# Kernel tuning notes

Measured on AMD Instinct MI355X. Metric: run time of the kernel, lower is better.

## Reference

```python
import jax, jax.numpy as jnp
import numpy as np

D_Z, D_X, K, T = 128, 64, 16, 2048
JITTER = 1e-4
# Tsit5 Butcher tableau. diffrax.diffeqsolve with the default ConstantStepSize
# controller and dt0 = t_curr - t_prev takes exactly ONE Tsit5 step per interval,
# so a single explicit Tsit5 step reproduces the original math.
A21 = 0.161
A31, A32 = -0.008480655492356989, 0.335480655492357
A41, A42, A43 = 2.8971530571054935, -6.359448489975075, 4.3622954328695815
A51, A52, A53, A54 = 5.325864828439257, -11.748883564062828, 7.4955393428898365, -0.09249506636175525
A61, A62, A63, A64, A65 = 5.86145544294642, -12.92096931784711, 8.159367898576159, -0.071584973281401, -0.028269050394068383
B1, B2, B3, B4, B5, B6 = 0.09646076681806523, 0.01, 0.4798896504144996, 1.379008574103742, -3.290069515436081, 2.324710524099774


def setup_inputs() -> dict:
    key = jax.random.key(0)
    ks = jax.random.split(key, 8)
    xs = jax.random.normal(ks[0], (T, D_X), jnp.float32)
    ts = jnp.arange(T, dtype=jnp.float32) * 0.01  # strictly increasing observation times
    expected_s = jax.nn.softmax(jax.random.normal(ks[1], (T, K), jnp.float32), axis=-1)
    mu_0 = jax.random.normal(ks[2], (D_Z,), jnp.float32)
    P_0 = jnp.eye(D_Z, dtype=jnp.float32)
    # stable continuous dynamics: small random part, negative diagonal shift
    A_s = 0.02 * jax.random.normal(ks[3], (K, D_Z, D_Z), jnp.float32) - 0.5 * jnp.eye(D_Z, dtype=jnp.float32)
    b_s = 0.1 * jax.random.normal(ks[4], (K, D_Z), jnp.float32)
    Q_s_chol = 0.1 + 0.1 * jax.random.uniform(ks[5], (K, D_Z), dtype=jnp.float32)
    C = jax.random.normal(ks[6], (D_X, D_Z), jnp.float32) / jnp.sqrt(jnp.float32(D_Z))
    R = 0.1 * jnp.eye(D_X, dtype=jnp.float32)
    return dict(xs=xs, ts=ts, expected_s=expected_s, mu_0=mu_0, P_0=P_0,
                A_s=A_s, b_s=b_s, Q_s_chol=Q_s_chol, C=C, R=R)


def _ode_func(state, s_prob, A_s, b_s, Q_s_chol):
    # state packs [mu (D_Z), P.flatten() (D_Z*D_Z)]
    mu, P = state[:D_Z], state[D_Z:].reshape(D_Z, D_Z)
    w = s_prob / jnp.sum(s_prob)  # jnp.average(..., weights=s_prob) semantics
    drift = jnp.einsum('k,kij,j->i', w, A_s, mu) + w @ b_s
    eA = jnp.einsum('k,kij->ij', w, A_s)
    eQ = jnp.diag(w @ (Q_s_chol ** 2))  # weighted avg of diag(Q_chol)^2
    dP = eA @ P + P @ eA.T + eQ
    return jnp.concatenate([drift, dP.reshape(-1)])


def _kf_update(mu, P, x, C, R):
    y = x - C @ mu
    S = C @ P @ C.T + R + JITTER * jnp.eye(R.shape[0], dtype=P.dtype)
    cho = jax.scipy.linalg.cho_factor(S)
    Kg = jax.scipy.linalg.cho_solve(cho, C @ P).T
    mu_u = mu + Kg @ y
    P_u = P - Kg @ C @ P
    return mu_u, 0.5 * (P_u + P_u.T)


def reference(xs, ts, expected_s, mu_0, P_0, A_s, b_s, Q_s_chol, C, R):
    mu0u, P0u = _kf_update(mu_0, P_0, xs[0], C, R)

    def step(carry, inp):
        mu_prev, P_prev, t_prev = carry
        x, t, s = inp
        y0 = jnp.concatenate([mu_prev, P_prev.reshape(-1)])
        f = lambda st: _ode_func(st, s, A_s, b_s, Q_s_chol)

        def integrate(_):
            h = t - t_prev
            k1 = f(y0)
            k2 = f(y0 + h * (A21 * k1))
            k3 = f(y0 + h * (A31 * k1 + A32 * k2))
            k4 = f(y0 + h * (A41 * k1 + A42 * k2 + A43 * k3))
            k5 = f(y0 + h * (A51 * k1 + A52 * k2 + A53 * k3 + A54 * k4))
            k6 = f(y0 + h * (A61 * k1 + A62 * k2 + A63 * k3 + A64 * k4 + A65 * k5))
            return y0 + h * (B1 * k1 + B2 * k2 + B3 * k3 + B4 * k4 + B5 * k5 + B6 * k6)

        state_pred = jax.lax.cond(t > t_prev, integrate, lambda _: y0, None)
        mu_pr, P_pr = state_pred[:D_Z], state_pred[D_Z:].reshape(D_Z, D_Z)
        mu_u, P_u = _kf_update(mu_pr, P_pr, x, C, R)
        return (mu_u, P_u, t), (mu_u, P_u)

    _, (mu_f, P_f) = jax.lax.scan(step, (mu0u, P0u, ts[0]), (xs[1:], ts[1:], expected_s[1:]))
    mu_filt = jnp.concatenate([mu0u[None], mu_f], axis=0)  # (T, D_Z)
    P_filt = jnp.concatenate([P0u[None], P_f], axis=0)  # (T, D_Z, D_Z)
    return mu_filt, P_filt
```

## Files before the change

### kernel.cpp

```cpp
#include <hip/hip_runtime.h>
#include <math.h>

#define DZ 128
#define DX 64
#define KMIX 16
#define JITTER_C 1e-4f
#define MS (DZ*DZ)
#define ESZ (4*MS + 2*DZ)
#define NCH 256
#define NT 1024
#define SCN (5*MS + 256)

#define SP   0
#define SX   (1*MS)
#define SX2  (2*MS)
#define SX2T (3*MS)
#define SQ   (4*MS)

template<int M, int N, int K, int MODE, bool DUAL>
__device__ void mm_(const float* __restrict__ At, const float* __restrict__ B,
                    float* __restrict__ out, const float* __restrict__ aux,
                    float* __restrict__ outT, float e1 = 0.f)
{
    __syncthreads();
    const int tid = threadIdx.x;
    constexpr int TM = M/32, TN = N/32;
    const int tx = tid & 31, ty = tid >> 5;
    const int i0 = ty*TM, j0 = tx*TN;
    float acc[TM*TN];
#pragma unroll
    for (int e = 0; e < TM*TN; ++e) acc[e] = 0.f;
#pragma unroll 8
    for (int k = 0; k < K; ++k) {
        const float* ar = At + k*M + i0;
        const float* br = B + k*N + j0;
        float av[TM], bv[TN];
        if constexpr (TM == 2) {
            float2 t = *reinterpret_cast<const float2*>(ar);
            av[0]=t.x; av[1]=t.y;
        } else {
#pragma unroll
            for (int a = 0; a < TM; a += 4) {
                float4 t = *reinterpret_cast<const float4*>(ar + a);
                av[a]=t.x; av[a+1]=t.y; av[a+2]=t.z; av[a+3]=t.w;
            }
        }
        if constexpr (TN == 2) {
            float2 t = *reinterpret_cast<const float2*>(br);
            bv[0]=t.x; bv[1]=t.y;
        } else {
#pragma unroll
            for (int b = 0; b < TN; b += 4) {
                float4 t = *reinterpret_cast<const float4*>(br + b);
                bv[b]=t.x; bv[b+1]=t.y; bv[b+2]=t.z; bv[b+3]=t.w;
            }
        }
#pragma unroll
        for (int a = 0; a < TM; ++a)
#pragma unroll
            for (int b = 0; b < TN; ++b)
                acc[a*TN+b] = fmaf(av[a], bv[b], acc[a*TN+b]);
    }
#pragma unroll
    for (int a = 0; a < TM; ++a) {
#pragma unroll
        for (int b = 0; b < TN; ++b) {
            const int row = i0+a, col = j0+b;
            const int idx = row*N + col;
            float v = acc[a*TN+b];
            if constexpr (MODE == 1) v += out[idx];
            else if constexpr (MODE == 2) v = aux[idx] - v;
            else if constexpr (MODE == 3) v += aux[idx];
            else if constexpr (MODE == 4) { v += e1*aux[idx]; if (row==col) v += 1.f; }
            out[idx] = v;
            acc[a*TN+b] = v;
        }
    }
    if constexpr (DUAL) {
#pragma unroll
        for (int b = 0; b < TN; ++b) {
#pragma unroll
            for (int a = 0; a < TM; a += 4) {
                float4 v = make_float4(acc[(a)*TN+b], acc[(a+1)*TN+b], acc[(a+2)*TN+b], acc[(a+3)*TN+b]);
                *reinterpret_cast<float4*>(outT + (j0+b)*M + i0 + a) = v;
            }
        }
    }
    __syncthreads();
}

template<int M, int K, int MODE>
__device__ void mv_(const float* __restrict__ At, const float* __restrict__ v,
                    float* __restrict__ out, const float* __restrict__ aux)
{
    __syncthreads();
    const int tid = threadIdx.x;
    if (tid < M) {
        float s = 0.f;
        for (int k = 0; k < K; ++k)
            s = fmaf(At[k*M + tid], v[k], s);
        float r;
        if constexpr (MODE == 0) r = s;
        else if constexpr (MODE == 1) r = aux[tid] + s;
        else r = aux[tid] - s;
        out[tid] = r;
    }
    __syncthreads();
}

__device__ void trans_g(const float* __restrict__ src, float* __restrict__ dst,
                        float* __restrict__ Lb)
{
    __syncthreads();
    for (int e = threadIdx.x; e < MS; e += NT) Lb[e] = src[e];
    __syncthreads();
    for (int e = threadIdx.x; e < MS; e += NT) {
        int j = e >> 7, i = e & 127;
        dst[e] = Lb[i*DZ + j];
    }
    __syncthreads();
}

__device__ void gj64_spd(float* __restrict__ A, float* __restrict__ st)
{
    const int tid = threadIdx.x;
    for (int p = 0; p < DX; p += 4) {
        __syncthreads();
        if (tid < 64) {
#pragma unroll
            for (int b = 0; b < 4; ++b) st[tid*4+b] = A[tid*DX + p + b];
        } else if (tid < 128) {
            int j = tid - 64;
#pragma unroll
            for (int b = 0; b < 4; ++b) st[256 + b*64 + j] = A[(p+b)*DX + j];
        }
        __syncthreads();
        float Dm[16], Di[16];
#pragma unroll
        for (int a = 0; a < 4; ++a)
#pragma unroll
            for (int b = 0; b < 4; ++b) {
                Dm[a*4+b] = st[(p+a)*4 + b];
                Di[a*4+b] = (a==b) ? 1.f : 0.f;
            }
#pragma unroll
        for (int q = 0; q < 4; ++q) {
            float rp = 1.f / Dm[q*4+q];
#pragma unroll
            for (int j = 0; j < 4; ++j) { Dm[q*4+j] *= rp; Di[q*4+j] *= rp; }
#pragma unroll
            for (int i = 0; i < 4; ++i) {
                if (i == q) continue;
                float f = Dm[i*4+q];
#pragma unroll
                for (int j = 0; j < 4; ++j) { Dm[i*4+j] = fmaf(-f, Dm[q*4+j], Dm[i*4+j]); Di[i*4+j] = fmaf(-f, Di[q*4+j], Di[i*4+j]); }
            }
        }
        for (int e = tid; e < DX*DX; e += NT) {
            const int i = e >> 6, j = e & 63;
            const bool iP = (i >= p) && (i < p+4);
            const bool jP = (j >= p) && (j < p+4);
            float o;
            if (iP && jP) {
                o = Di[(i-p)*4 + (j-p)];
            } else if (iP) {
                const int a = i - p;
                o = Di[a*4+0]*st[256+0*64+j] + Di[a*4+1]*st[256+1*64+j]
                  + Di[a*4+2]*st[256+2*64+j] + Di[a*4+3]*st[256+3*64+j];
            } else {
                float Ei[4];
#pragma unroll
                for (int b = 0; b < 4; ++b)
                    Ei[b] = st[i*4+0]*Di[0*4+b] + st[i*4+1]*Di[1*4+b]
                          + st[i*4+2]*Di[2*4+b] + st[i*4+3]*Di[3*4+b];
                if (jP) o = -Ei[j-p];
                else    o = A[e] - (Ei[0]*st[256+0*64+j] + Ei[1]*st[256+1*64+j]
                                  + Ei[2]*st[256+2*64+j] + Ei[3]*st[256+3*64+j]);
            }
            A[e] = o;
        }
    }
    __syncthreads();
}

__device__ void gj128_piv(float* __restrict__ A, float* __restrict__ pc, float* __restrict__ pr,
                          int* __restrict__ rec, int* __restrict__ ipv1)
{
    __syncthreads();
    const int tid = threadIdx.x;
    for (int p = 0; p < DZ; ++p) {
        if (tid < 64) {
            float best = -1.f; int bi = p;
            for (int i = tid; i < DZ; i += 64) {
                float v = (i >= p) ? fabsf(A[i*DZ + p]) : -2.f;
                if (v > best) { best = v; bi = i; }
            }
            for (int off = 32; off > 0; off >>= 1) {
                float ob = __shfl_xor(best, off);
                int obi = __shfl_xor(bi, off);
                if (ob > best) { best = ob; bi = obi; }
            }
            if (tid == 0) { rec[p] = bi; ipv1[0] = bi; }
        }
        __syncthreads();
        const int r = ipv1[0];
        if (r != p) {
            for (int j = tid; j < DZ; j += NT) { float t = A[p*DZ+j]; A[p*DZ+j] = A[r*DZ+j]; A[r*DZ+j] = t; }
            __syncthreads();
        }
        if (tid < DZ) { pc[tid] = A[tid*DZ + p]; pr[tid] = A[p*DZ + tid]; }
        __syncthreads();
        const float rp = 1.f / pr[p];
        for (int e = tid; e < MS; e += NT) {
            const int i = e >> 7, j = e & 127;
            const float pv = pr[j] * rp;
            float o;
            if (i == p) o = (j == p) ? rp : pv;
            else { const float fc = pc[i]; o = (j == p) ? (-fc*rp) : (A[e] - fc*pv); }
            A[e] = o;
        }
        __syncthreads();
    }
    for (int p = DZ - 1; p >= 0; --p) {
        const int r = rec[p];
        if (r != p) {
            for (int i = tid; i < DZ; i += NT) { float t = A[i*DZ+p]; A[i*DZ+p] = A[i*DZ+r]; A[i*DZ+r] = t; }
            __syncthreads();
        }
    }
    __syncthreads();
}

__device__ void phase1_dev(int k,
    const float* __restrict__ A_s, const float* __restrict__ b_s,
    const float* __restrict__ Qch, const float* __restrict__ es, const float* __restrict__ ts,
    float* sx, float* sx2, float* sx2t, float* sq,
    float* L0, float* L1,
    float* W16, float* ebv, float* eqv, float* vvv, float* cvec,
    float g1, float g2, float g3, float g4)
{
    const int tid = threadIdx.x;
    const float h = ts[k] - ts[k-1];
    if (h <= 0.f) {
        __syncthreads();
        for (int e = tid; e < MS; e += NT) {
            int i = e >> 7, j = e & 127;
            L0[e] = (i==j) ? 1.f : 0.f;
            sq[e] = 0.f;
        }
        if (tid < DZ) cvec[tid] = 0.f;
        __syncthreads();
        return;
    }
    __syncthreads();
    if (tid < KMIX) W16[tid] = es[(size_t)k*KMIX + tid];
    __syncthreads();
    if (tid == 0) {
        float s = 0.f;
        for (int m = 0; m < KMIX; ++m) s += W16[m];
        float inv = 1.f/s;
        for (int m = 0; m < KMIX; ++m) W16[m] *= inv;
    }
    __syncthreads();
    if (tid < DZ) {
        float eb = 0.f, eq = 0.f;
        for (int m = 0; m < KMIX; ++m) {
            float wm = W16[m];
            eb = fmaf(wm, b_s[m*DZ+tid], eb);
            float qc = Qch[m*DZ+tid];
            eq = fmaf(wm, qc*qc, eq);
        }
        ebv[tid] = eb; eqv[tid] = eq;
    }
    const int tx = tid & 31, ty = tid >> 5;
    const int i0 = ty*4, j0 = tx*4;
    float t16[16];
#pragma unroll
    for (int e = 0; e < 16; ++e) t16[e] = 0.f;
    for (int m = 0; m < KMIX; ++m) {
        float wm = W16[m];
        const float* Am = A_s + (size_t)m * MS;
#pragma unroll
        for (int a = 0; a < 4; ++a) {
            float4 p0 = *reinterpret_cast<const float4*>(&Am[(i0+a)*DZ + j0]);
            t16[a*4+0]=fmaf(wm,p0.x,t16[a*4+0]); t16[a*4+1]=fmaf(wm,p0.y,t16[a*4+1]);
            t16[a*4+2]=fmaf(wm,p0.z,t16[a*4+2]); t16[a*4+3]=fmaf(wm,p0.w,t16[a*4+3]);
        }
    }
#pragma unroll
    for (int a = 0; a < 4; ++a)
#pragma unroll
        for (int b = 0; b < 4; ++b) {
            float v = h * t16[a*4+b];
            L1[(i0+a)*DZ + (j0+b)] = v;
            sx[(i0+a)*DZ + (j0+b)] = v;
            L0[(j0+b)*DZ + (i0+a)] = v;
        }
    __syncthreads();
    {
        float gg[5]; gg[1]=g1; gg[2]=g2; gg[3]=g3; gg[4]=g4;
        if (tid < DZ) vvv[tid] = ebv[tid];
        float creg = (tid < DZ) ? g1 * ebv[tid] : 0.f;
        __syncthreads();
        for (int m = 1; m <= 3; ++m) {
            float vn = 0.f;
            if (tid < DZ)
                for (int kk = 0; kk < DZ; ++kk)
                    vn = fmaf(L0[kk*DZ + tid], vvv[kk], vn);
            __syncthreads();
            if (tid < DZ) vvv[tid] = vn;
            creg = fmaf(gg[m+1], vn, creg);
            __syncthreads();
        }
        if (tid < DZ) cvec[tid] = h * creg;
    }
    mm_<128,128,128,0,true>(L0, L1, sx2, nullptr, sx2t);
    for (int e = tid; e < MS; e += NT) {
        int j = e >> 7, i = e & 127;
        float xt = L0[e];
        float w1  = g2*sx[e] + g3*sx2[e];
        float w1t = g2*xt    + g3*sx2t[e];
        float vq = w1*eqv[i] + eqv[j]*w1t;
        if (i == j) vq += g1*eqv[j];
        sq[e] = h * vq;
        L1[e] = g3*xt + ((i==j) ? g2 : 0.f);
    }
    __syncthreads();
    mm_<128,128,128,4,false>(sx2, L1, L0, L0, nullptr, g1);
}

#define SHARED_DECLS \
    __shared__ __align__(16) float L0[MS]; \
    __shared__ __align__(16) float L1[MS]; \
    __shared__ __align__(16) float SL[DX*DX]; \
    __shared__ __align__(16) float GJB[520]; \
    __shared__ float V0[DZ],V1[DZ],V2[DZ],V3[DZ],V4[DZ],V5[DZ]; \
    __shared__ float r64s[DX], u64s[DX]; \
    __shared__ float W16[KMIX], ebv[DZ], eqv[DZ], vvv[DZ], cvec[DZ]; \
    __shared__ float GJc[DZ], GJr[DZ]; \
    __shared__ int REC[DZ]; __shared__ int IPV1[1];

__global__ __launch_bounds__(NT) void kf_prep(
    const float* __restrict__ Cm, const float* __restrict__ Rm,
    const float* __restrict__ mu0, const float* __restrict__ P0,
    const float* __restrict__ xs,
    float* Ct, float* Rj, float* Rji, float* mu0u, float* p0u, float* scr)
{
    SHARED_DECLS
    const int tid = threadIdx.x;
    for (int i = tid; i < DZ*DX; i += NT) { int z = i>>6, m = i&63; Ct[i] = Cm[m*DZ + z]; }
    for (int i = tid; i < DX*DX; i += NT) {
        int a = i>>6, b = i&63;
        float v = Rm[i] + ((a==b) ? JITTER_C : 0.f);
        Rj[i] = v; SL[i] = v;
    }
    gj64_spd(SL, GJB);
    for (int i = tid; i < DX*DX; i += NT) Rji[i] = SL[i];
    float* z  = scr + SX;
    float* cp = scr + SX + DZ*DX;
    float* kt = scr + SX2;
    mm_<128,64,128,0,true>(P0, Ct, z, nullptr, cp);
    mm_<64,64,128,3,false>(Ct, z, SL, Rj, nullptr);
    gj64_spd(SL, GJB);
    mm_<64,128,64,0,false>(SL, cp, kt, nullptr, nullptr);
    mv_<64,128,2>(Ct, mu0, r64s, xs);
    mv_<128,64,1>(kt, r64s, mu0u, mu0);
    mm_<128,128,64,2,false>(kt, cp, p0u, P0, nullptr);
    __syncthreads();
    for (int e = tid; e < MS; e += NT) L0[e] = p0u[e];
    __syncthreads();
    for (int e = tid; e < MS; e += NT) {
        int i = e>>7, j = e&127;
        p0u[e] = 0.5f * (L0[e] + L0[j*DZ + i]);
    }
}

__global__ __launch_bounds__(NT) void kf_passA(
    const float* __restrict__ A_s, const float* __restrict__ b_s,
    const float* __restrict__ Qch, const float* __restrict__ es,
    const float* __restrict__ ts, const float* __restrict__ xs,
    const float* __restrict__ Ct, const float* __restrict__ Rj,
    const float* __restrict__ Rji,
    const float* __restrict__ mu0u, const float* __restrict__ p0u,
    float* elems, float* scr, int T, int LCH,
    float g1, float g2, float g3, float g4)
{
    SHARED_DECLS
    const int c = blockIdx.x, tid = threadIdx.x;
    float* sc = scr + (size_t)c * SCN;
    float* R = elems + (size_t)c * ESZ;
    float* RAs = R; float* RAts = R+MS; float* RCs = R+2*MS; float* RJs = R+3*MS;
    float* Rbs = R+4*MS; float* Rhs = R+4*MS+DZ;
    int eBeg = c*LCH, eEnd = (c*LCH + LCH < T) ? (c*LCH + LCH) : T;
    if (eBeg >= eEnd && c != 0) {
        for (int e = tid; e < MS; e += NT) {
            int i = e>>7, j = e&127; float id = (i==j)?1.f:0.f;
            RAs[e]=id; RAts[e]=id; RCs[e]=0.f; RJs[e]=0.f;
        }
        if (tid < DZ) { Rbs[tid]=0.f; Rhs[tid]=0.f; }
        return;
    }
    if (c == 0) {
        for (int e = tid; e < MS; e += NT) { RAs[e]=0.f; RCs[e]=p0u[e]; RJs[e]=0.f; }
        if (tid < DZ) { V0[tid]=mu0u[tid]; V5[tid]=0.f; }
        eBeg = 1;
    } else {
        for (int e = tid; e < MS; e += NT) {
            int i = e>>7, j = e&127;
            RAs[e] = (i==j)?1.f:0.f; RCs[e]=0.f; RJs[e]=0.f;
        }
        if (tid < DZ) { V0[tid]=0.f; V5[tid]=0.f; }
    }
    __syncthreads();
    float* sx = sc+SX; float* sx2 = sc+SX2; float* sx2t = sc+SX2T; float* sq = sc+SQ;
    float* z  = L0;    float* zt = L0 + 8192;
    float* y  = sq;    float* hh = sq + 8192;
    float* h2 = sx;
    for (int e = eBeg; e < eEnd; ++e) {
        phase1_dev(e, A_s,b_s,Qch,es,ts, sx,sx2,sx2t,sq, L0,L1,
                   W16,ebv,eqv,vvv,cvec, g1,g2,g3,g4);
        mm_<128,128,128,0,false>(L0, RAs, sx, nullptr, nullptr);
        mv_<128,128,1>(L0, V0, V1, cvec);
        mm_<128,128,128,0,false>(RCs, L0, sx2, nullptr, nullptr);
        mm_<128,128,128,3,false>(L0, sx2, L1, sq, nullptr);
        mm_<128,64,128,0,true>(L1, Ct, z, nullptr, zt);
        mm_<64,64,128,3,false>(Ct, z, SL, Rj, nullptr);
        gj64_spd(SL, GJB);
        mm_<64,128,128,0,false>(Ct, sx, y, nullptr, nullptr);
        mm_<64,128,64,0,false>(SL, y, hh, nullptr, nullptr);
        mm_<128,128,64,2,false>(zt, hh, RAs, sx, nullptr);
        mm_<128,128,64,1,false>(y, hh, RJs, nullptr, nullptr);
        mm_<64,128,64,0,false>(SL, zt, h2, nullptr, nullptr);
        mm_<128,128,64,2,false>(zt, h2, RCs, L1, nullptr);
        mv_<64,128,2>(Ct, V1, r64s, xs + (size_t)e*DX);
        mv_<64,64,0>(Rji, xs + (size_t)e*DX, u64s, nullptr);
        mv_<128,64,1>(zt, u64s, V2, V1);
        mv_<64,128,0>(Ct, V2, GJc, nullptr);
        mv_<64,64,0>(SL, GJc, GJr, nullptr);
        mv_<128,64,2>(zt, GJr, V0, V2);
        mv_<64,64,0>(SL, r64s, u64s, nullptr);
        mv_<128,64,1>(y, u64s, V5, V5);
    }
    __syncthreads();
    if (tid < DZ) { Rbs[tid] = V0[tid]; Rhs[tid] = V5[tid]; }
    trans_g(RAs, RAts, L0);
}

__device__ void combine(float* Rd,
    const float* EA, const float* EAt, const float* EC, const float* EJ,
    const float* Ebg, const float* Ehg,
    float* t2, float* t3,
    float* L0, float* L1,
    float* V0, float* V1, float* V2, float* V3, float* V4, float* V5,
    float* GJc, float* GJr, int* REC, int* IPV1, int lastj)
{
    float* RA = Rd; float* RAt = Rd+MS; float* RC = Rd+2*MS; float* RJ = Rd+3*MS;
    float* Rb = Rd+4*MS; float* Rh = Rd+4*MS+DZ;
    const int tid = threadIdx.x;
    __syncthreads();
    if (tid < DZ) { V0[tid]=Ebg[tid]; V1[tid]=Ehg[tid]; V2[tid]=Rb[tid]; }
    mm_<128,128,128,0,false>(EJ, RC, L0, nullptr, nullptr);
    if (tid < DZ) L0[tid*DZ + tid] += 1.f;
    gj128_piv(L0, GJc, GJr, REC, IPV1);
    if (!lastj) {
        mm_<128,128,128,0,false>(L0, RA, L1, nullptr, nullptr);
        mm_<128,128,128,0,false>(EJ, RA, t2, nullptr, nullptr);
        mm_<128,128,128,1,false>(L1, t2, RJ, nullptr, nullptr);
        mv_<128,128,2>(EJ, V2, V4, V1);
        mv_<128,128,1>(L1, V4, Rh, Rh);
    }
    mv_<128,128,1>(RC, V1, V3, V2);
    mv_<128,128,0>(L0, V3, V5, nullptr);
    mv_<128,128,1>(EAt, V5, Rb, V0);
    mm_<128,128,128,0,false>(L0, RC, t3, nullptr, nullptr);
    mm_<128,128,128,0,false>(t3, EAt, t2, nullptr, nullptr);
    mm_<128,128,128,3,false>(EAt, t2, RC, EC, nullptr);
    if (!lastj) {
        mm_<128,128,128,0,false>(EAt, L1, RA, nullptr, nullptr);
        trans_g(RA, RAt, L1);
    }
}

__global__ __launch_bounds__(NT) void kf_scan(
    const float* __restrict__ in, float* __restrict__ out, float* scr, int r, int lastj)
{
    SHARED_DECLS
    const int c = blockIdx.x;
    float* sc = scr + (size_t)c * SCN;
    float* dst = out + (size_t)c * ESZ;
    const float* src = in + (size_t)((c >= r) ? (c - r) : c) * ESZ;
    if (lastj) {
        for (int e = threadIdx.x; e < MS; e += NT) dst[2*MS + e] = src[2*MS + e];
        for (int e = threadIdx.x; e < DZ; e += NT) dst[4*MS + e] = src[4*MS + e];
    } else {
        for (int e = threadIdx.x; e < ESZ; e += NT) dst[e] = src[e];
    }
    if (c >= r) {
        const float* E = in + (size_t)c * ESZ;
        combine(dst, E, E+MS, E+2*MS, E+3*MS, E+4*MS, E+4*MS+DZ,
                sc+SP, sc+SX, L0, L1,
                V0,V1,V2,V3,V4,V5, GJc, GJr, REC, IPV1, lastj);
    }
}

__global__ __launch_bounds__(NT) void kf_passC(
    const float* __restrict__ A_s, const float* __restrict__ b_s,
    const float* __restrict__ Qch, const float* __restrict__ es,
    const float* __restrict__ ts, const float* __restrict__ xs,
    const float* __restrict__ Ct, const float* __restrict__ Rj,
    const float* __restrict__ mu0u, const float* __restrict__ p0u,
    const float* __restrict__ pfx,
    float* mu_out, float* P_out, float* scr, int T, int LCH,
    float g1, float g2, float g3, float g4)
{
    SHARED_DECLS
    const int c = blockIdx.x, tid = threadIdx.x;
    float* sc = scr + (size_t)c * SCN;
    float* P = sc + SP;
    int eBeg = c*LCH, eEnd = (c*LCH + LCH < T) ? (c*LCH + LCH) : T;
    if (eBeg >= eEnd && c != 0) return;
    if (c == 0) {
        for (int e = tid; e < MS; e += NT) { float v = p0u[e]; P[e] = v; P_out[e] = v; }
        if (tid < DZ) { V0[tid] = mu0u[tid]; mu_out[tid] = mu0u[tid]; }
        eBeg = 1;
    } else {
        const float* X = pfx + (size_t)(c-1) * ESZ;
        for (int e = tid; e < MS; e += NT) P[e] = X[2*MS + e];
        if (tid < DZ) V0[tid] = X[4*MS + tid];
    }
    __syncthreads();
    float* sx = sc+SX; float* sx2 = sc+SX2; float* sx2t = sc+SX2T; float* sq = sc+SQ;
    float* z  = L0;    float* zt = L0 + 8192;
    for (int e = eBeg; e < eEnd; ++e) {
        phase1_dev(e, A_s,b_s,Qch,es,ts, sx,sx2,sx2t,sq, L0,L1,
                   W16,ebv,eqv,vvv,cvec, g1,g2,g3,g4);
        mm_<128,128,128,0,false>(P, L0, sx, nullptr, nullptr);
        mm_<128,128,128,3,false>(L0, sx, L1, sq, nullptr);
        mv_<128,128,1>(L0, V0, V1, cvec);
        mm_<128,64,128,0,true>(L1, Ct, z, nullptr, zt);
        mm_<64,64,128,3,false>(Ct, z, SL, Rj, nullptr);
        gj64_spd(SL, GJB);
        mm_<64,128,64,0,false>(SL, zt, sx2, nullptr, nullptr);
        mv_<64,128,2>(Ct, V1, r64s, xs + (size_t)e*DX);
        mv_<128,64,1>(sx2, r64s, V0, V1);
        if (tid < DZ) mu_out[(size_t)e*DZ + tid] = V0[tid];
        mm_<128,128,64,2,false>(zt, sx2, L1, L1, nullptr);
        float* po = P_out + (size_t)e * MS;
        for (int ee = tid; ee < MS; ee += NT) {
            int i = ee>>7, j = ee&127;
            float v = 0.5f * (L1[ee] + L1[j*DZ + i]);
            P[ee] = v;
            __builtin_nontemporal_store(v, &po[ee]);
        }
        __syncthreads();
    }
}

static void compute_gamma(double g[7])
{
    const double A[6][5] = {
        {0, 0, 0, 0, 0},
        {0.161, 0, 0, 0, 0},
        {-0.008480655492356989, 0.335480655492357, 0, 0, 0},
        {2.8971530571054935, -6.359448489975075, 4.3622954328695815, 0, 0},
        {5.325864828439257, -11.748883564062828, 7.4955393428898365, -0.09249506636175525, 0},
        {5.86145544294642, -12.92096931784711, 8.159367898576159, -0.071584973281401, -0.028269050394068383}};
    const double B[6] = {0.09646076681806523, 0.01, 0.4798896504144996,
                         1.379008574103742, -3.290069515436081, 2.324710524099774};
    double e[6][6];
    for (int i = 0; i < 6; ++i)
        for (int d = 0; d < 6; ++d) e[i][d] = 0.0;
    for (int i = 0; i < 6; ++i) {
        e[i][0] = 1.0;
        for (int j = 0; j < i; ++j)
            for (int d = 0; d < 5; ++d)
                e[i][d + 1] += A[i][j] * e[j][d];
    }
    g[0] = 1.0;
    for (int m = 1; m <= 6; ++m) {
        double s = 0.0;
        for (int i = 0; i < 6; ++i) s += B[i] * e[i][m - 1];
        g[m] = s;
    }
}

extern "C" void kernel_launch(void* const* d_in, const int* in_sizes, int n_in,
                              void* d_out, int out_size, void* d_ws, size_t ws_size,
                              hipStream_t stream)
{
    const float* xs  = (const float*)d_in[0];
    const float* ts  = (const float*)d_in[1];
    const float* es  = (const float*)d_in[2];
    const float* mu0 = (const float*)d_in[3];
    const float* P0  = (const float*)d_in[4];
    const float* A_s = (const float*)d_in[5];
    const float* b_s = (const float*)d_in[6];
    const float* Qch = (const float*)d_in[7];
    const float* Cm  = (const float*)d_in[8];
    const float* Rm  = (const float*)d_in[9];
    const int T = in_sizes[1];

    float* mu_out = (float*)d_out;
    float* P_out  = mu_out + (size_t)T * DZ;

    float* ws = (float*)d_ws;
    float* Ct    = ws;
    float* Rj    = ws + 8192;
    float* Rji   = ws + 12288;
    float* mu0u  = ws + 16384;
    float* p0u   = ws + 16512;
    float* elemsA = ws + 32896;
    float* elemsB = elemsA + (size_t)NCH * ESZ;
    float* scr    = elemsB + (size_t)NCH * ESZ;

    const int LCH = (T + NCH - 1) / NCH;

    double g[7];
    compute_gamma(g);
    const float g1 = (float)g[1], g2 = (float)g[2], g3 = (float)g[3], g4 = (float)g[4];

    hipLaunchKernelGGL(kf_prep, dim3(1), dim3(NT), 0, stream,
                       Cm, Rm, mu0, P0, xs, Ct, Rj, Rji, mu0u, p0u, scr);
    hipLaunchKernelGGL(kf_passA, dim3(NCH), dim3(NT), 0, stream,
                       A_s, b_s, Qch, es, ts, xs, Ct, Rj, Rji, mu0u, p0u,
                       elemsA, scr, T, LCH, g1, g2, g3, g4);
    float* bufs[2] = {elemsA, elemsB};
    int cur = 0;
    for (int r = 1; r < NCH; r <<= 1) {
        const int lastj = ((r << 1) >= NCH) ? 1 : 0;
        hipLaunchKernelGGL(kf_scan, dim3(NCH), dim3(NT), 0, stream,
                           bufs[cur], bufs[cur ^ 1], scr, r, lastj);
        cur ^= 1;
    }
    hipLaunchKernelGGL(kf_passC, dim3(NCH), dim3(NT), 0, stream,
                       A_s, b_s, Qch, es, ts, xs, Ct, Rj, mu0u, p0u,
                       bufs[cur], mu_out, P_out, scr, T, LCH, g1, g2, g3, g4);
}
```

Before: 11.93 ms.

## Reduce LDS bank conflicts in matmul, matvec, transpose and symmetrization

```diff
diff --git a/kernel.cpp b/kernel.cpp
--- a/kernel.cpp
+++ b/kernel.cpp
@@ -30,8 +30,7 @@
     float acc[TM*TN];
 #pragma unroll
     for (int e = 0; e < TM*TN; ++e) acc[e] = 0.f;
-#pragma unroll 8
-    for (int k = 0; k < K; ++k) {
+    auto body = [&](int k) {
         const float* ar = At + k*M + i0;
         const float* br = B + k*N + j0;
         float av[TM], bv[TN];
@@ -60,7 +59,12 @@
 #pragma unroll
             for (int b = 0; b < TN; ++b)
                 acc[a*TN+b] = fmaf(av[a], bv[b], acc[a*TN+b]);
-    }
+    };
+    const int off = (tid >> 6) * (K >> 4);
+#pragma unroll 8
+    for (int k = off; k < K; ++k) body(k);
+#pragma unroll 8
+    for (int k = 0; k < off; ++k) body(k);
 #pragma unroll
     for (int a = 0; a < TM; ++a) {
 #pragma unroll
@@ -95,15 +99,23 @@
 {
     __syncthreads();
     const int tid = threadIdx.x;
-    if (tid < M) {
-        float s = 0.f;
-        for (int k = 0; k < K; ++k)
-            s = fmaf(At[k*M + tid], v[k], s);
-        float r;
-        if constexpr (MODE == 0) r = s;
-        else if constexpr (MODE == 1) r = aux[tid] + s;
-        else r = aux[tid] - s;
-        out[tid] = r;
+    constexpr int TPR = NT / M;
+    constexpr int CH  = K / TPR;
+    const int r  = tid / TPR;
+    const int sg = tid % TPR;
+    const int k0 = sg * CH;
+    float s = 0.f;
+#pragma unroll
+    for (int k = 0; k < CH; ++k)
+        s = fmaf(At[(k0 + k)*M + r], v[k0 + k], s);
+#pragma unroll
+    for (int o = 1; o < TPR; o <<= 1) s += __shfl_xor(s, o);
+    if (sg == 0) {
+        float rr;
+        if constexpr (MODE == 0) rr = s;
+        else if constexpr (MODE == 1) rr = aux[r] + s;
+        else rr = aux[r] - s;
+        out[r] = rr;
     }
     __syncthreads();
 }
@@ -112,11 +124,14 @@
                         float* __restrict__ Lb)
 {
     __syncthreads();
-    for (int e = threadIdx.x; e < MS; e += NT) Lb[e] = src[e];
-    __syncthreads();
     for (int e = threadIdx.x; e < MS; e += NT) {
-        int j = e >> 7, i = e & 127;
-        dst[e] = Lb[i*DZ + j];
+        int i = e >> 7, j = e & 127;
+        Lb[(i << 7) + (j ^ (i & 31))] = src[e];
+    }
+    __syncthreads();
+    for (int e = threadIdx.x; e < MS; e += NT) {
+        int a = e >> 7, b = e & 127;
+        dst[e] = Lb[(b << 7) + (a ^ (b & 31))];
     }
     __syncthreads();
 }
@@ -277,14 +292,18 @@
     float t16[16];
 #pragma unroll
     for (int e = 0; e < 16; ++e) t16[e] = 0.f;
-    for (int m = 0; m < KMIX; ++m) {
-        float wm = W16[m];
-        const float* Am = A_s + (size_t)m * MS;
-#pragma unroll
-        for (int a = 0; a < 4; ++a) {
-            float4 p0 = *reinterpret_cast<const float4*>(&Am[(i0+a)*DZ + j0]);
-            t16[a*4+0]=fmaf(wm,p0.x,t16[a*4+0]); t16[a*4+1]=fmaf(wm,p0.y,t16[a*4+1]);
-            t16[a*4+2]=fmaf(wm,p0.z,t16[a*4+2]); t16[a*4+3]=fmaf(wm,p0.w,t16[a*4+3]);
+    {
+        const int mq = (tid >> 6) & (KMIX - 1);
+        for (int mi = 0; mi < KMIX; ++mi) {
+            int m = mi + mq; if (m >= KMIX) m -= KMIX;
+            float wm = W16[m];
+            const float* Am = A_s + (size_t)m * MS;
+#pragma unroll
+            for (int a = 0; a < 4; ++a) {
+                float4 p0 = *reinterpret_cast<const float4*>(&Am[(i0+a)*DZ + j0]);
+                t16[a*4+0]=fmaf(wm,p0.x,t16[a*4+0]); t16[a*4+1]=fmaf(wm,p0.y,t16[a*4+1]);
+                t16[a*4+2]=fmaf(wm,p0.z,t16[a*4+2]); t16[a*4+3]=fmaf(wm,p0.w,t16[a*4+3]);
+            }
         }
     }
 #pragma unroll
@@ -545,10 +564,15 @@
         mv_<128,64,1>(sx2, r64s, V0, V1);
         if (tid < DZ) mu_out[(size_t)e*DZ + tid] = V0[tid];
         mm_<128,128,64,2,false>(zt, sx2, L1, L1, nullptr);
+        for (int ee = tid; ee < MS; ee += NT) {
+            int i = ee >> 7, j = ee & 127;
+            L0[(i << 7) + (j ^ (i & 31))] = L1[ee];
+        }
+        __syncthreads();
         float* po = P_out + (size_t)e * MS;
         for (int ee = tid; ee < MS; ee += NT) {
-            int i = ee>>7, j = ee&127;
-            float v = 0.5f * (L1[ee] + L1[j*DZ + i]);
+            int i = ee >> 7, j = ee & 127;
+            float v = 0.5f * (L1[ee] + L0[(j << 7) + (i ^ (j & 31))]);
             P[ee] = v;
             __builtin_nontemporal_store(v, &po[ee]);
         }
```

Measured after the change: 11.66 ms. -2.2%, faster.
